# Kernel optimization log

Hardware: AMD Instinct MI355X
Metric: run time of the kernel (lower is better)

## Reference

```python
import jax, jax.numpy as jnp
import numpy as np

T, B, D_IN, H = 1024, 64, 256, 256
D_CAT = D_IN + H  # input to each gate MLP


def setup_inputs() -> dict:
    key = jax.random.key(0)
    k_x, k_w1, k_w2 = jax.random.split(key, 3)
    inputs = jax.random.normal(k_x, (T, B, D_IN), dtype=jnp.float32)
    # 4 gates (forget, input, update, output), weights stacked on leading axis.
    # Layout: W1[g] is (in, out) so combined @ W1[g] + b1[g].
    W1 = jax.random.normal(k_w1, (4, D_CAT, H), dtype=jnp.float32) * (1.0 / np.sqrt(D_CAT))
    b1 = jnp.zeros((4, H), dtype=jnp.float32)
    W2 = jax.random.normal(k_w2, (4, H, H), dtype=jnp.float32) * (1.0 / np.sqrt(H))
    b2 = jnp.zeros((4, H), dtype=jnp.float32)
    return {"inputs": inputs, "W1": W1, "b1": b1, "W2": W2, "b2": b2}


def reference(inputs, W1, b1, W2, b2):
    """HybridQLSTM forward. inputs: [T, B, D_IN]. Returns (stacked [T,B,H], (hx, cx))."""
    Bsz = inputs.shape[1]
    h0 = jnp.zeros((Bsz, H), dtype=inputs.dtype)
    c0 = jnp.zeros((Bsz, H), dtype=inputs.dtype)

    def step(carry, x):
        hx, cx = carry
        combined = jnp.concatenate([x, hx], axis=1)  # [B, D_CAT]
        # All 4 gate MLPs at once: sigmoid(W2 @ tanh(W1 @ combined + b1) + b2)
        hid = jnp.tanh(jnp.einsum('bd,gdh->gbh', combined, W1) + b1[:, None, :])
        gates = jax.nn.sigmoid(jnp.einsum('gbh,ghk->gbk', hid, W2) + b2[:, None, :])
        f, i, u, o = gates[0], gates[1], gates[2], gates[3]
        g = jnp.tanh(u)  # faithful: tanh applied on top of sampler sigmoid
        cx = f * cx + i * g
        hx = o * jnp.tanh(cx)
        return (hx, cx), hx

    (hx, cx), stacked = jax.lax.scan(step, (h0, c0), inputs)
    return stacked, (hx, cx)
```

## Files before the change

### kernel.cpp

```cpp
#include <hip/hip_runtime.h>
#include <math.h>


#define TS    1024
#define NELEM 16384

typedef unsigned long long u64;
typedef unsigned int u32;
typedef unsigned short u16;
typedef _Float16 f16;
typedef __attribute__((ext_vector_type(8))) _Float16 half8;
typedef __attribute__((ext_vector_type(8))) unsigned short ushort8;
typedef __attribute__((ext_vector_type(4))) float f32x4;

__device__ __forceinline__ u64 ld_a8(const u64* p) {
    return __hip_atomic_load(p, __ATOMIC_RELAXED, __HIP_MEMORY_SCOPE_AGENT);
}
__device__ __forceinline__ void st_a8(u64* p, u64 v) {
    __hip_atomic_store(p, v, __ATOMIC_RELAXED, __HIP_MEMORY_SCOPE_AGENT);
}
__device__ __forceinline__ void st_a2(u16* p, u16 v) {
    __hip_atomic_store(p, v, __ATOMIC_RELAXED, __HIP_MEMORY_SCOPE_AGENT);
}

__device__ __forceinline__ void gbar(int e, int bid, int tid, int* flags) {
    __syncthreads();
    if (tid == 0)
        __hip_atomic_store(&flags[bid * 16], e, __ATOMIC_RELAXED, __HIP_MEMORY_SCOPE_AGENT);
    const int l = tid & 63;
    for (;;) {
        int ok = 1;
        if (l < 16) {
            int v = __hip_atomic_load(&flags[l * 16], __ATOMIC_RELAXED, __HIP_MEMORY_SCOPE_AGENT);
            ok = (v >= e);
        }
        if (__all(ok)) break;
        __builtin_amdgcn_s_sleep(1);
    }
    asm volatile("" ::: "memory");
}

__device__ __forceinline__ half8 h8_from(u64 v0, u64 v1) {
    ushort8 t;
#pragma unroll
    for (int q = 0; q < 4; ++q) {
        t[q]     = (u16)(v0 >> (16 * q));
        t[4 + q] = (u16)(v1 >> (16 * q));
    }
    return __builtin_bit_cast(half8, t);
}

__global__ __launch_bounds__(256) void qinit(u64* hglob, int* flags) {
    int i = blockIdx.x * 256 + threadIdx.x;
    st_a8(&hglob[i], 0ull);
    if (i < 16 * 16)
        __hip_atomic_store(&flags[i], 0, __ATOMIC_RELAXED, __HIP_MEMORY_SCOPE_AGENT);
}

__global__ __launch_bounds__(256, 1) void qlstm_persist(
    const float* __restrict__ x,
    const float* __restrict__ W1,
    const float* __restrict__ b1,
    const float* __restrict__ W2,
    const float* __restrict__ b2,
    float* __restrict__ out,
    u64* __restrict__ hglob,
    u16* __restrict__ hidg,
    u16* __restrict__ gateq,
    int* __restrict__ flags)
{
    const int tid = threadIdx.x;
    const int bid = blockIdx.x;
    const int g  = bid >> 2;
    const int ct = bid & 3;

    __shared__ f16 w1s[16 * 4 * 512];
    __shared__ f16 w2s[8 * 4 * 512];
    {
        const float* W1g = W1 + (size_t)g * 512 * 256;
        for (int i = tid; i < 16 * 4 * 64; i += 256) {
            int kt = i >> 8, nt = (i >> 6) & 3, lane = i & 63;
            int k0 = kt * 32 + (lane >> 4) * 8;
            int col = ct * 64 + nt * 16 + (lane & 15);
#pragma unroll
            for (int j = 0; j < 8; ++j)
                w1s[((kt * 4 + nt) * 64 + lane) * 8 + j] = (f16)W1g[(size_t)(k0 + j) * 256 + col];
        }
        const float* W2g = W2 + (size_t)g * 256 * 256;
        for (int i = tid; i < 8 * 4 * 64; i += 256) {
            int kt = i >> 8, nt = (i >> 6) & 3, lane = i & 63;
            int k0 = kt * 32 + (lane >> 4) * 8;
            int col = ct * 64 + nt * 16 + (lane & 15);
#pragma unroll
            for (int j = 0; j < 8; ++j)
                w2s[((kt * 4 + nt) * 64 + lane) * 8 + j] = (f16)W2g[(size_t)(k0 + j) * 256 + col];
        }
        __syncthreads();
    }

    const int l    = tid & 63;
    const int w    = tid >> 6;
    const int quad = l >> 4;
    const int n15  = l & 15;
    const int brow = w * 16 + n15;
    const int bo   = w * 16 + quad * 4;
    float b1v[4], b2v[4];
#pragma unroll
    for (int nt = 0; nt < 4; ++nt) {
        b1v[nt] = b1[g * 256 + ct * 64 + nt * 16 + n15];
        b2v[nt] = b2[g * 256 + ct * 64 + nt * 16 + n15];
    }
    const int e0   = bid * 1024 + tid * 4;
    const int urow = e0 >> 8;
    const int ucol = e0 & 255;
    float creg[4] = {0.f, 0.f, 0.f, 0.f};

    f32x4 acc[4];
#pragma unroll
    for (int nt = 0; nt < 4; ++nt) acc[nt] = (f32x4){0.f, 0.f, 0.f, 0.f};

    {
        const float* xr = x + (size_t)brow * 256;
#pragma unroll
        for (int kt = 0; kt < 8; ++kt) {
            float a[8];
            *(float4*)&a[0] = *(const float4*)(xr + kt * 32 + quad * 8);
            *(float4*)&a[4] = *(const float4*)(xr + kt * 32 + quad * 8 + 4);
            half8 ah;
#pragma unroll
            for (int j = 0; j < 8; ++j) ah[j] = (f16)a[j];
#pragma unroll
            for (int nt = 0; nt < 4; ++nt)
                acc[nt] = __builtin_amdgcn_mfma_f32_16x16x32_f16(
                    ah, *(const half8*)&w1s[((kt * 4 + nt) * 64 + l) * 8], acc[nt], 0, 0, 0);
        }
    }

    for (int t = 0; t < TS; ++t) {
        {
            const u64* hp = hglob + brow * 64;
#pragma unroll
            for (int kt = 8; kt < 16; ++kt) {
                int ko = (kt - 8) * 8 + quad * 2;
                u64 v0 = ld_a8(hp + ko);
                u64 v1 = ld_a8(hp + ko + 1);
                half8 ah = h8_from(v0, v1);
#pragma unroll
                for (int nt = 0; nt < 4; ++nt)
                    acc[nt] = __builtin_amdgcn_mfma_f32_16x16x32_f16(
                        ah, *(const half8*)&w1s[((kt * 4 + nt) * 64 + l) * 8], acc[nt], 0, 0, 0);
            }
        }
#pragma unroll
        for (int nt = 0; nt < 4; ++nt)
#pragma unroll
            for (int r = 0; r < 4; ++r) {
                f16 v = (f16)tanhf(acc[nt][r] + b1v[nt]);
                st_a2(&hidg[(size_t)(g * 64 + bo + r) * 256 + ct * 64 + nt * 16 + n15],
                      __builtin_bit_cast(u16, v));
            }

        gbar(3 * t + 1, bid, tid, flags);

        {
            f32x4 s2[4];
#pragma unroll
            for (int nt = 0; nt < 4; ++nt) s2[nt] = (f32x4){0.f, 0.f, 0.f, 0.f};
            const u64* hr = (const u64*)(hidg + (size_t)(g * 64 + brow) * 256);
#pragma unroll
            for (int kt = 0; kt < 8; ++kt) {
                int ko = kt * 8 + quad * 2;
                u64 v0 = ld_a8(hr + ko);
                u64 v1 = ld_a8(hr + ko + 1);
                half8 ah = h8_from(v0, v1);
#pragma unroll
                for (int nt = 0; nt < 4; ++nt)
                    s2[nt] = __builtin_amdgcn_mfma_f32_16x16x32_f16(
                        ah, *(const half8*)&w2s[((kt * 4 + nt) * 64 + l) * 8], s2[nt], 0, 0, 0);
            }
#pragma unroll
            for (int nt = 0; nt < 4; ++nt)
#pragma unroll
                for (int r = 0; r < 4; ++r) {
                    float sg = 1.0f / (1.0f + expf(-(s2[nt][r] + b2v[nt])));
                    st_a2(&gateq[(size_t)(g * 64 + bo + r) * 256 + ct * 64 + nt * 16 + n15],
                          (u16)(sg * 65535.0f + 0.5f));
                }
        }

        gbar(3 * t + 2, bid, tid, flags);

        {
            const u16* gq = gateq + urow * 256 + ucol;
            u64 qf = ld_a8((const u64*)(gq));
            u64 qi = ld_a8((const u64*)(gq + 16384));
            u64 qu = ld_a8((const u64*)(gq + 32768));
            u64 qo = ld_a8((const u64*)(gq + 49152));
            float4 ov;
            u64 hpack = 0;
            const float s = 1.0f / 65535.0f;
#pragma unroll
            for (int k = 0; k < 4; ++k) {
                float f = (float)((qf >> (16 * k)) & 0xffff) * s;
                float i = (float)((qi >> (16 * k)) & 0xffff) * s;
                float u = (float)((qu >> (16 * k)) & 0xffff) * s;
                float o = (float)((qo >> (16 * k)) & 0xffff) * s;
                creg[k] = f * creg[k] + i * tanhf(u);
                float hn = o * tanhf(creg[k]);
                ((float*)&ov)[k] = hn;
                u16 hb = __builtin_bit_cast(u16, (f16)hn);
                hpack |= (u64)hb << (16 * k);
            }
            *(float4*)(out + (size_t)t * NELEM + e0) = ov;
            st_a8(&hglob[e0 >> 2], hpack);
            if (t == TS - 1) {
                *(float4*)(out + (size_t)TS * NELEM + e0) = ov;
                float4 cv = {creg[0], creg[1], creg[2], creg[3]};
                *(float4*)(out + (size_t)TS * NELEM + NELEM + e0) = cv;
            }
        }

#pragma unroll
        for (int nt = 0; nt < 4; ++nt) acc[nt] = (f32x4){0.f, 0.f, 0.f, 0.f};
        if (t < TS - 1) {
            const float* xr = x + ((size_t)(t + 1) * 64 + brow) * 256;
#pragma unroll
            for (int kt = 0; kt < 8; ++kt) {
                float a[8];
                *(float4*)&a[0] = *(const float4*)(xr + kt * 32 + quad * 8);
                *(float4*)&a[4] = *(const float4*)(xr + kt * 32 + quad * 8 + 4);
                half8 ah;
#pragma unroll
                for (int j = 0; j < 8; ++j) ah[j] = (f16)a[j];
#pragma unroll
                for (int nt = 0; nt < 4; ++nt)
                    acc[nt] = __builtin_amdgcn_mfma_f32_16x16x32_f16(
                        ah, *(const half8*)&w1s[((kt * 4 + nt) * 64 + l) * 8], acc[nt], 0, 0, 0);
            }
        }

        gbar(3 * t + 3, bid, tid, flags);
    }
}

extern "C" void kernel_launch(void* const* d_in, const int* in_sizes, int n_in,
                              void* d_out, int out_size, void* d_ws, size_t ws_size,
                              hipStream_t stream)
{
    const float* x  = (const float*)d_in[0];
    const float* W1 = (const float*)d_in[1];
    const float* b1 = (const float*)d_in[2];
    const float* W2 = (const float*)d_in[3];
    const float* b2 = (const float*)d_in[4];
    float* out = (float*)d_out;

    char* ws = (char*)d_ws;
    u64* hglob = (u64*)ws;
    u16* hidg  = (u16*)(ws + 32768);
    u16* gateq = (u16*)(ws + 32768 + 131072);
    int* flags = (int*)(ws + 32768 + 131072 + 131072);

    qinit<<<16, 256, 0, stream>>>(hglob, flags);
    qlstm_persist<<<16, 256, 0, stream>>>(x, W1, b1, W2, b2, out,
                                          hglob, hidg, gateq, flags);
}
```

Before: 13.43 ms.

## Replace global flag barriers with tagged data words and double-buffered exchange

Removes the three per-step grid-wide flag barriers and instead packs a 16-bit timestep tag into each 64-bit exchanged word. Consumers spin on the data itself until every tag matches. Hidden, gate and h buffers are double-buffered by timestep parity, so producers can run ahead without a trailing barrier. It also switches to fast exp/rcp-based tanh and sigmoid and moves the tanh on the update gate into the producer. The costs are more bytes per exchange (tag overhead) and heavier polling traffic, plus reduced transcendental accuracy.

```diff
diff --git a/kernel.cpp b/kernel.cpp
--- a/kernel.cpp
+++ b/kernel.cpp
@@ -10,7 +10,6 @@
 typedef unsigned short u16;
 typedef _Float16 f16;
 typedef __attribute__((ext_vector_type(8))) _Float16 half8;
-typedef __attribute__((ext_vector_type(8))) unsigned short ushort8;
 typedef __attribute__((ext_vector_type(4))) float f32x4;
 
 __device__ __forceinline__ u64 ld_a8(const u64* p) {
@@ -19,42 +18,19 @@
 __device__ __forceinline__ void st_a8(u64* p, u64 v) {
     __hip_atomic_store(p, v, __ATOMIC_RELAXED, __HIP_MEMORY_SCOPE_AGENT);
 }
-__device__ __forceinline__ void st_a2(u16* p, u16 v) {
-    __hip_atomic_store(p, v, __ATOMIC_RELAXED, __HIP_MEMORY_SCOPE_AGENT);
-}
-
-__device__ __forceinline__ void gbar(int e, int bid, int tid, int* flags) {
-    __syncthreads();
-    if (tid == 0)
-        __hip_atomic_store(&flags[bid * 16], e, __ATOMIC_RELAXED, __HIP_MEMORY_SCOPE_AGENT);
-    const int l = tid & 63;
-    for (;;) {
-        int ok = 1;
-        if (l < 16) {
-            int v = __hip_atomic_load(&flags[l * 16], __ATOMIC_RELAXED, __HIP_MEMORY_SCOPE_AGENT);
-            ok = (v >= e);
-        }
-        if (__all(ok)) break;
-        __builtin_amdgcn_s_sleep(1);
-    }
-    asm volatile("" ::: "memory");
-}
-
-__device__ __forceinline__ half8 h8_from(u64 v0, u64 v1) {
-    ushort8 t;
-#pragma unroll
-    for (int q = 0; q < 4; ++q) {
-        t[q]     = (u16)(v0 >> (16 * q));
-        t[4 + q] = (u16)(v1 >> (16 * q));
-    }
-    return __builtin_bit_cast(half8, t);
-}
-
-__global__ __launch_bounds__(256) void qinit(u64* hglob, int* flags) {
-    int i = blockIdx.x * 256 + threadIdx.x;
-    st_a8(&hglob[i], 0ull);
-    if (i < 16 * 16)
-        __hip_atomic_store(&flags[i], 0, __ATOMIC_RELAXED, __HIP_MEMORY_SCOPE_AGENT);
+
+__device__ __forceinline__ float fast_tanh(float xx) {
+    float e = __expf(2.0f * xx);
+    return 1.0f - 2.0f * __builtin_amdgcn_rcpf(e + 1.0f);
+}
+__device__ __forceinline__ float fast_sig(float xx) {
+    return __builtin_amdgcn_rcpf(1.0f + __expf(-xx));
+}
+
+__global__ __launch_bounds__(256) void qinit(u64* ws64, int n) {
+    int stride = gridDim.x * 256;
+    for (int i = blockIdx.x * 256 + threadIdx.x; i < n; i += stride)
+        st_a8(&ws64[i], 0ull);
 }
 
 __global__ __launch_bounds__(256, 1) void qlstm_persist(
@@ -64,10 +40,9 @@
     const float* __restrict__ W2,
     const float* __restrict__ b2,
     float* __restrict__ out,
-    u64* __restrict__ hglob,
-    u16* __restrict__ hidg,
-    u16* __restrict__ gateq,
-    int* __restrict__ flags)
+    u64* __restrict__ h64,
+    u64* __restrict__ hid64,
+    u64* __restrict__ gat64)
 {
     const int tid = threadIdx.x;
     const int bid = blockIdx.x;
@@ -138,81 +113,141 @@
 
     for (int t = 0; t < TS; ++t) {
         {
-            const u64* hp = hglob + brow * 64;
-#pragma unroll
-            for (int kt = 8; kt < 16; ++kt) {
-                int ko = (kt - 8) * 8 + quad * 2;
-                u64 v0 = ld_a8(hp + ko);
-                u64 v1 = ld_a8(hp + ko + 1);
-                half8 ah = h8_from(v0, v1);
+            const u64* hb = h64 + (size_t)(t & 1) * 8192 + (size_t)brow * 128;
+            const u16 wantH = (u16)t;
+            u64 hv[32];
+            for (;;) {
+                bool ok = true;
+#pragma unroll
+                for (int i = 0; i < 32; ++i) {
+                    int kt = i >> 2, j = i & 3;
+                    hv[i] = ld_a8(hb + kt * 16 + quad * 4 + j);
+                }
+#pragma unroll
+                for (int i = 0; i < 32; ++i) ok &= ((u16)(hv[i] >> 48) == wantH);
+                if (__all(ok)) break;
+            }
+#pragma unroll
+            for (int kt = 0; kt < 8; ++kt) {
+                half8 ah;
+#pragma unroll
+                for (int j = 0; j < 4; ++j) {
+                    u64 v = hv[kt * 4 + j];
+                    ah[2 * j]     = __builtin_bit_cast(f16, (u16)v);
+                    ah[2 * j + 1] = __builtin_bit_cast(f16, (u16)(v >> 32));
+                }
 #pragma unroll
                 for (int nt = 0; nt < 4; ++nt)
                     acc[nt] = __builtin_amdgcn_mfma_f32_16x16x32_f16(
-                        ah, *(const half8*)&w1s[((kt * 4 + nt) * 64 + l) * 8], acc[nt], 0, 0, 0);
-            }
-        }
-#pragma unroll
-        for (int nt = 0; nt < 4; ++nt)
-#pragma unroll
-            for (int r = 0; r < 4; ++r) {
-                f16 v = (f16)tanhf(acc[nt][r] + b1v[nt]);
-                st_a2(&hidg[(size_t)(g * 64 + bo + r) * 256 + ct * 64 + nt * 16 + n15],
-                      __builtin_bit_cast(u16, v));
-            }
-
-        gbar(3 * t + 1, bid, tid, flags);
+                        ah, *(const half8*)&w1s[(((kt + 8) * 4 + nt) * 64 + l) * 8], acc[nt], 0, 0, 0);
+            }
+        }
+
+        {
+            u64* hd = hid64 + (size_t)(t & 1) * 32768;
+            const u64 tagw = (u64)(u16)(t + 1) << 48;
+#pragma unroll
+            for (int nt = 0; nt < 4; ++nt)
+#pragma unroll
+                for (int r = 0; r < 4; ++r) {
+                    f16 v = (f16)fast_tanh(acc[nt][r] + b1v[nt]);
+                    u32 pv = (u32)__builtin_bit_cast(u16, v);
+                    u32 po = (u32)__shfl_xor((int)pv, 1);
+                    if ((n15 & 1) == 0) {
+                        int cp = ct * 32 + nt * 8 + (n15 >> 1);
+                        st_a8(&hd[(size_t)(g * 64 + bo + r) * 128 + cp],
+                              tagw | ((u64)po << 32) | pv);
+                    }
+                }
+        }
 
         {
             f32x4 s2[4];
 #pragma unroll
             for (int nt = 0; nt < 4; ++nt) s2[nt] = (f32x4){0.f, 0.f, 0.f, 0.f};
-            const u64* hr = (const u64*)(hidg + (size_t)(g * 64 + brow) * 256);
+            const u64* hr = hid64 + (size_t)(t & 1) * 32768 + (size_t)(g * 64 + brow) * 128;
+            const u16 wantM = (u16)(t + 1);
+            u64 mv[32];
+            for (;;) {
+                bool ok = true;
+#pragma unroll
+                for (int i = 0; i < 32; ++i) {
+                    int kt = i >> 2, j = i & 3;
+                    mv[i] = ld_a8(hr + kt * 16 + quad * 4 + j);
+                }
+#pragma unroll
+                for (int i = 0; i < 32; ++i) ok &= ((u16)(mv[i] >> 48) == wantM);
+                if (__all(ok)) break;
+            }
 #pragma unroll
             for (int kt = 0; kt < 8; ++kt) {
-                int ko = kt * 8 + quad * 2;
-                u64 v0 = ld_a8(hr + ko);
-                u64 v1 = ld_a8(hr + ko + 1);
-                half8 ah = h8_from(v0, v1);
+                half8 ah;
+#pragma unroll
+                for (int j = 0; j < 4; ++j) {
+                    u64 v = mv[kt * 4 + j];
+                    ah[2 * j]     = __builtin_bit_cast(f16, (u16)v);
+                    ah[2 * j + 1] = __builtin_bit_cast(f16, (u16)(v >> 32));
+                }
 #pragma unroll
                 for (int nt = 0; nt < 4; ++nt)
                     s2[nt] = __builtin_amdgcn_mfma_f32_16x16x32_f16(
                         ah, *(const half8*)&w2s[((kt * 4 + nt) * 64 + l) * 8], s2[nt], 0, 0, 0);
             }
+            u64* gd = gat64 + (size_t)(t & 1) * 32768;
+            const u64 tagw = (u64)(u16)(t + 1) << 48;
 #pragma unroll
             for (int nt = 0; nt < 4; ++nt)
 #pragma unroll
                 for (int r = 0; r < 4; ++r) {
-                    float sg = 1.0f / (1.0f + expf(-(s2[nt][r] + b2v[nt])));
-                    st_a2(&gateq[(size_t)(g * 64 + bo + r) * 256 + ct * 64 + nt * 16 + n15],
-                          (u16)(sg * 65535.0f + 0.5f));
-                }
-        }
-
-        gbar(3 * t + 2, bid, tid, flags);
-
-        {
-            const u16* gq = gateq + urow * 256 + ucol;
-            u64 qf = ld_a8((const u64*)(gq));
-            u64 qi = ld_a8((const u64*)(gq + 16384));
-            u64 qu = ld_a8((const u64*)(gq + 32768));
-            u64 qo = ld_a8((const u64*)(gq + 49152));
+                    float sg = fast_sig(s2[nt][r] + b2v[nt]);
+                    if (g == 2) sg = fast_tanh(sg);
+                    u32 q  = (u32)(sg * 65535.0f + 0.5f);
+                    u32 oq = (u32)__shfl_xor((int)q, 1);
+                    if ((n15 & 1) == 0) {
+                        int cp = ct * 32 + nt * 8 + (n15 >> 1);
+                        st_a8(&gd[(size_t)(g * 64 + bo + r) * 128 + cp],
+                              tagw | ((u64)oq << 16) | q);
+                    }
+                }
+        }
+
+        {
+            const u64* gb = gat64 + (size_t)(t & 1) * 32768 + (size_t)urow * 128 + (ucol >> 1);
+            const u16 wantG = (u16)(t + 1);
+            u64 gv[8];
+            for (;;) {
+                bool ok = true;
+#pragma unroll
+                for (int gg = 0; gg < 4; ++gg) {
+                    gv[gg * 2]     = ld_a8(gb + gg * 8192);
+                    gv[gg * 2 + 1] = ld_a8(gb + gg * 8192 + 1);
+                }
+#pragma unroll
+                for (int i = 0; i < 8; ++i) ok &= ((u16)(gv[i] >> 48) == wantG);
+                if (__all(ok)) break;
+            }
             float4 ov;
-            u64 hpack = 0;
             const float s = 1.0f / 65535.0f;
+            u64* hw = h64 + (size_t)((t + 1) & 1) * 8192;
+            const u64 tagH = (u64)(u16)(t + 1) << 48;
+            u64 hp[2];
 #pragma unroll
             for (int k = 0; k < 4; ++k) {
-                float f = (float)((qf >> (16 * k)) & 0xffff) * s;
-                float i = (float)((qi >> (16 * k)) & 0xffff) * s;
-                float u = (float)((qu >> (16 * k)) & 0xffff) * s;
-                float o = (float)((qo >> (16 * k)) & 0xffff) * s;
-                creg[k] = f * creg[k] + i * tanhf(u);
-                float hn = o * tanhf(creg[k]);
+                int wsel = k >> 1, sh = 16 * (k & 1);
+                float f  = (float)((gv[0 + wsel] >> sh) & 0xffff) * s;
+                float i  = (float)((gv[2 + wsel] >> sh) & 0xffff) * s;
+                float gu = (float)((gv[4 + wsel] >> sh) & 0xffff) * s;
+                float o  = (float)((gv[6 + wsel] >> sh) & 0xffff) * s;
+                creg[k] = f * creg[k] + i * gu;
+                float hn = o * fast_tanh(creg[k]);
                 ((float*)&ov)[k] = hn;
-                u16 hb = __builtin_bit_cast(u16, (f16)hn);
-                hpack |= (u64)hb << (16 * k);
+                u64 hb16 = (u64)__builtin_bit_cast(u16, (f16)hn);
+                if ((k & 1) == 0) hp[k >> 1] = tagH | hb16;
+                else              hp[k >> 1] |= (hb16 << 32);
             }
             *(float4*)(out + (size_t)t * NELEM + e0) = ov;
-            st_a8(&hglob[e0 >> 2], hpack);
+            st_a8(&hw[urow * 128 + (ucol >> 1)],     hp[0]);
+            st_a8(&hw[urow * 128 + (ucol >> 1) + 1], hp[1]);
             if (t == TS - 1) {
                 *(float4*)(out + (size_t)TS * NELEM + e0) = ov;
                 float4 cv = {creg[0], creg[1], creg[2], creg[3]};
@@ -238,8 +273,6 @@
                         ah, *(const half8*)&w1s[((kt * 4 + nt) * 64 + l) * 8], acc[nt], 0, 0, 0);
             }
         }
-
-        gbar(3 * t + 3, bid, tid, flags);
     }
 }
 
@@ -255,12 +288,11 @@
     float* out = (float*)d_out;
 
     char* ws = (char*)d_ws;
-    u64* hglob = (u64*)ws;
-    u16* hidg  = (u16*)(ws + 32768);
-    u16* gateq = (u16*)(ws + 32768 + 131072);
-    int* flags = (int*)(ws + 32768 + 131072 + 131072);
-
-    qinit<<<16, 256, 0, stream>>>(hglob, flags);
+    u64* h64   = (u64*)ws;
+    u64* hid64 = (u64*)(ws + 131072);
+    u64* gat64 = (u64*)(ws + 131072 + 524288);
+
+    qinit<<<64, 256, 0, stream>>>((u64*)ws, 147456);
     qlstm_persist<<<16, 256, 0, stream>>>(x, W1, b1, W2, b2, out,
-                                          hglob, hidg, gateq, flags);
-}
+                                          h64, hid64, gat64);
+}
```

After: 23.97 ms. 78.5% more time.

## Repartition blocks by hidden column across all gates to drop one grid barrier per step

Applied to the files above, without the earlier changes.

Each of the 16 blocks now owns 16 hidden columns for all four gates instead of 64 columns of one gate. The LSTM cell update can then run right after the second MLP layer without a global exchange of quantized gate values, so each timestep needs two grid barriers instead of three. Hidden activations are transposed in-register with shuffles and stored as packed 64-bit words, and the second-layer loads are batched before the MFMAs. tanh and sigmoid use fast exp/rcp approximations, and the 16-bit gate quantization is removed, with some small accuracy tradeoffs.

```diff
diff --git a/kernel.cpp b/kernel.cpp
--- a/kernel.cpp
+++ b/kernel.cpp
@@ -19,8 +19,13 @@
 __device__ __forceinline__ void st_a8(u64* p, u64 v) {
     __hip_atomic_store(p, v, __ATOMIC_RELAXED, __HIP_MEMORY_SCOPE_AGENT);
 }
-__device__ __forceinline__ void st_a2(u16* p, u16 v) {
-    __hip_atomic_store(p, v, __ATOMIC_RELAXED, __HIP_MEMORY_SCOPE_AGENT);
+
+__device__ __forceinline__ float fast_tanh(float xx) {
+    float e = __expf(2.0f * xx);
+    return 1.0f - 2.0f * __builtin_amdgcn_rcpf(e + 1.0f);
+}
+__device__ __forceinline__ float fast_sig(float xx) {
+    return __builtin_amdgcn_rcpf(1.0f + __expf(-xx));
 }
 
 __device__ __forceinline__ void gbar(int e, int bid, int tid, int* flags) {
@@ -50,11 +55,33 @@
     return __builtin_bit_cast(half8, t);
 }
 
-__global__ __launch_bounds__(256) void qinit(u64* hglob, int* flags) {
+__device__ __forceinline__ void xpose4(float v[4], int p) {
+#pragma unroll
+    for (int m = 1; m <= 2; m <<= 1) {
+        float nv[4];
+#pragma unroll
+        for (int r = 0; r < 4; ++r) {
+            float ex = __shfl_xor(v[r ^ m], m);
+            nv[r] = ((r ^ p) & m) ? ex : v[r];
+        }
+#pragma unroll
+        for (int r = 0; r < 4; ++r) v[r] = nv[r];
+    }
+}
+
+__device__ __forceinline__ u64 pk4f16(const float v[4]) {
+    u64 r = 0;
+#pragma unroll
+    for (int k = 0; k < 4; ++k)
+        r |= (u64)__builtin_bit_cast(u16, (f16)v[k]) << (16 * k);
+    return r;
+}
+
+__global__ __launch_bounds__(256) void qinit(u64* h64, int* flags) {
     int i = blockIdx.x * 256 + threadIdx.x;
-    st_a8(&hglob[i], 0ull);
-    if (i < 16 * 16)
-        __hip_atomic_store(&flags[i], 0, __ATOMIC_RELAXED, __HIP_MEMORY_SCOPE_AGENT);
+    st_a8(&h64[i], 0ull);
+    if (i < 128)
+        st_a8((u64*)flags + i, 0ull);
 }
 
 __global__ __launch_bounds__(256, 1) void qlstm_persist(
@@ -64,36 +91,34 @@
     const float* __restrict__ W2,
     const float* __restrict__ b2,
     float* __restrict__ out,
-    u64* __restrict__ hglob,
-    u16* __restrict__ hidg,
-    u16* __restrict__ gateq,
+    u64* __restrict__ h64,
+    u64* __restrict__ hid64,
     int* __restrict__ flags)
 {
     const int tid = threadIdx.x;
     const int bid = blockIdx.x;
-    const int g  = bid >> 2;
-    const int ct = bid & 3;
+    const int ct = bid;
 
     __shared__ f16 w1s[16 * 4 * 512];
     __shared__ f16 w2s[8 * 4 * 512];
     {
-        const float* W1g = W1 + (size_t)g * 512 * 256;
         for (int i = tid; i < 16 * 4 * 64; i += 256) {
-            int kt = i >> 8, nt = (i >> 6) & 3, lane = i & 63;
+            int kt = i >> 8, g = (i >> 6) & 3, lane = i & 63;
             int k0 = kt * 32 + (lane >> 4) * 8;
-            int col = ct * 64 + nt * 16 + (lane & 15);
+            int col = ct * 16 + (lane & 15);
+            const float* W1g = W1 + (size_t)g * 512 * 256;
 #pragma unroll
             for (int j = 0; j < 8; ++j)
-                w1s[((kt * 4 + nt) * 64 + lane) * 8 + j] = (f16)W1g[(size_t)(k0 + j) * 256 + col];
-        }
-        const float* W2g = W2 + (size_t)g * 256 * 256;
+                w1s[(size_t)i * 8 + j] = (f16)W1g[(size_t)(k0 + j) * 256 + col];
+        }
         for (int i = tid; i < 8 * 4 * 64; i += 256) {
-            int kt = i >> 8, nt = (i >> 6) & 3, lane = i & 63;
+            int kt = i >> 8, g = (i >> 6) & 3, lane = i & 63;
             int k0 = kt * 32 + (lane >> 4) * 8;
-            int col = ct * 64 + nt * 16 + (lane & 15);
+            int col = ct * 16 + (lane & 15);
+            const float* W2g = W2 + (size_t)g * 256 * 256;
 #pragma unroll
             for (int j = 0; j < 8; ++j)
-                w2s[((kt * 4 + nt) * 64 + lane) * 8 + j] = (f16)W2g[(size_t)(k0 + j) * 256 + col];
+                w2s[(size_t)i * 8 + j] = (f16)W2g[(size_t)(k0 + j) * 256 + col];
         }
         __syncthreads();
     }
@@ -104,20 +129,20 @@
     const int n15  = l & 15;
     const int brow = w * 16 + n15;
     const int bo   = w * 16 + quad * 4;
+    const int p    = l & 3;
+    const int cq   = ct * 4 + (n15 >> 2);
+    const int cbase = ct * 16 + (n15 & ~3);
     float b1v[4], b2v[4];
 #pragma unroll
-    for (int nt = 0; nt < 4; ++nt) {
-        b1v[nt] = b1[g * 256 + ct * 64 + nt * 16 + n15];
-        b2v[nt] = b2[g * 256 + ct * 64 + nt * 16 + n15];
-    }
-    const int e0   = bid * 1024 + tid * 4;
-    const int urow = e0 >> 8;
-    const int ucol = e0 & 255;
+    for (int g = 0; g < 4; ++g) {
+        b1v[g] = b1[g * 256 + ct * 16 + n15];
+        b2v[g] = b2[g * 256 + ct * 16 + n15];
+    }
     float creg[4] = {0.f, 0.f, 0.f, 0.f};
 
     f32x4 acc[4];
 #pragma unroll
-    for (int nt = 0; nt < 4; ++nt) acc[nt] = (f32x4){0.f, 0.f, 0.f, 0.f};
+    for (int g = 0; g < 4; ++g) acc[g] = (f32x4){0.f, 0.f, 0.f, 0.f};
 
     {
         const float* xr = x + (size_t)brow * 256;
@@ -130,98 +155,92 @@
 #pragma unroll
             for (int j = 0; j < 8; ++j) ah[j] = (f16)a[j];
 #pragma unroll
-            for (int nt = 0; nt < 4; ++nt)
-                acc[nt] = __builtin_amdgcn_mfma_f32_16x16x32_f16(
-                    ah, *(const half8*)&w1s[((kt * 4 + nt) * 64 + l) * 8], acc[nt], 0, 0, 0);
+            for (int g = 0; g < 4; ++g)
+                acc[g] = __builtin_amdgcn_mfma_f32_16x16x32_f16(
+                    ah, *(const half8*)&w1s[((kt * 4 + g) * 64 + l) * 8], acc[g], 0, 0, 0);
         }
     }
 
     for (int t = 0; t < TS; ++t) {
         {
-            const u64* hp = hglob + brow * 64;
-#pragma unroll
-            for (int kt = 8; kt < 16; ++kt) {
-                int ko = (kt - 8) * 8 + quad * 2;
-                u64 v0 = ld_a8(hp + ko);
-                u64 v1 = ld_a8(hp + ko + 1);
-                half8 ah = h8_from(v0, v1);
-#pragma unroll
-                for (int nt = 0; nt < 4; ++nt)
-                    acc[nt] = __builtin_amdgcn_mfma_f32_16x16x32_f16(
-                        ah, *(const half8*)&w1s[((kt * 4 + nt) * 64 + l) * 8], acc[nt], 0, 0, 0);
-            }
-        }
-#pragma unroll
-        for (int nt = 0; nt < 4; ++nt)
-#pragma unroll
-            for (int r = 0; r < 4; ++r) {
-                f16 v = (f16)tanhf(acc[nt][r] + b1v[nt]);
-                st_a2(&hidg[(size_t)(g * 64 + bo + r) * 256 + ct * 64 + nt * 16 + n15],
-                      __builtin_bit_cast(u16, v));
-            }
-
-        gbar(3 * t + 1, bid, tid, flags);
-
-        {
-            f32x4 s2[4];
-#pragma unroll
-            for (int nt = 0; nt < 4; ++nt) s2[nt] = (f32x4){0.f, 0.f, 0.f, 0.f};
-            const u64* hr = (const u64*)(hidg + (size_t)(g * 64 + brow) * 256);
+            const u64* hp = h64 + (size_t)brow * 64;
+            u64 hv[16];
 #pragma unroll
             for (int kt = 0; kt < 8; ++kt) {
                 int ko = kt * 8 + quad * 2;
-                u64 v0 = ld_a8(hr + ko);
-                u64 v1 = ld_a8(hr + ko + 1);
-                half8 ah = h8_from(v0, v1);
-#pragma unroll
-                for (int nt = 0; nt < 4; ++nt)
-                    s2[nt] = __builtin_amdgcn_mfma_f32_16x16x32_f16(
-                        ah, *(const half8*)&w2s[((kt * 4 + nt) * 64 + l) * 8], s2[nt], 0, 0, 0);
-            }
-#pragma unroll
-            for (int nt = 0; nt < 4; ++nt)
-#pragma unroll
-                for (int r = 0; r < 4; ++r) {
-                    float sg = 1.0f / (1.0f + expf(-(s2[nt][r] + b2v[nt])));
-                    st_a2(&gateq[(size_t)(g * 64 + bo + r) * 256 + ct * 64 + nt * 16 + n15],
-                          (u16)(sg * 65535.0f + 0.5f));
+                hv[kt * 2]     = ld_a8(hp + ko);
+                hv[kt * 2 + 1] = ld_a8(hp + ko + 1);
+            }
+#pragma unroll
+            for (int kt = 0; kt < 8; ++kt) {
+                half8 ah = h8_from(hv[kt * 2], hv[kt * 2 + 1]);
+#pragma unroll
+                for (int g = 0; g < 4; ++g)
+                    acc[g] = __builtin_amdgcn_mfma_f32_16x16x32_f16(
+                        ah, *(const half8*)&w1s[(((kt + 8) * 4 + g) * 64 + l) * 8], acc[g], 0, 0, 0);
+            }
+        }
+
+#pragma unroll
+        for (int g = 0; g < 4; ++g) {
+            float mv[4];
+#pragma unroll
+            for (int r = 0; r < 4; ++r) mv[r] = fast_tanh(acc[g][r] + b1v[g]);
+            xpose4(mv, p);
+            st_a8(&hid64[(size_t)(g * 64 + bo + p) * 64 + cq], pk4f16(mv));
+        }
+
+        gbar(2 * t + 1, bid, tid, flags);
+
+        f32x4 s2[4];
+#pragma unroll
+        for (int g = 0; g < 4; ++g) s2[g] = (f32x4){0.f, 0.f, 0.f, 0.f};
+        {
+            u64 mv[64];
+#pragma unroll
+            for (int kt = 0; kt < 8; ++kt)
+#pragma unroll
+                for (int g = 0; g < 4; ++g) {
+                    const u64* hr = hid64 + (size_t)(g * 64 + brow) * 64 + kt * 8 + quad * 2;
+                    mv[(kt * 4 + g) * 2]     = ld_a8(hr);
+                    mv[(kt * 4 + g) * 2 + 1] = ld_a8(hr + 1);
                 }
-        }
-
-        gbar(3 * t + 2, bid, tid, flags);
+#pragma unroll
+            for (int kt = 0; kt < 8; ++kt)
+#pragma unroll
+                for (int g = 0; g < 4; ++g) {
+                    half8 ah = h8_from(mv[(kt * 4 + g) * 2], mv[(kt * 4 + g) * 2 + 1]);
+                    s2[g] = __builtin_amdgcn_mfma_f32_16x16x32_f16(
+                        ah, *(const half8*)&w2s[((kt * 4 + g) * 64 + l) * 8], s2[g], 0, 0, 0);
+                }
+        }
 
         {
-            const u16* gq = gateq + urow * 256 + ucol;
-            u64 qf = ld_a8((const u64*)(gq));
-            u64 qi = ld_a8((const u64*)(gq + 16384));
-            u64 qu = ld_a8((const u64*)(gq + 32768));
-            u64 qo = ld_a8((const u64*)(gq + 49152));
-            float4 ov;
-            u64 hpack = 0;
-            const float s = 1.0f / 65535.0f;
-#pragma unroll
-            for (int k = 0; k < 4; ++k) {
-                float f = (float)((qf >> (16 * k)) & 0xffff) * s;
-                float i = (float)((qi >> (16 * k)) & 0xffff) * s;
-                float u = (float)((qu >> (16 * k)) & 0xffff) * s;
-                float o = (float)((qo >> (16 * k)) & 0xffff) * s;
-                creg[k] = f * creg[k] + i * tanhf(u);
-                float hn = o * tanhf(creg[k]);
-                ((float*)&ov)[k] = hn;
-                u16 hb = __builtin_bit_cast(u16, (f16)hn);
-                hpack |= (u64)hb << (16 * k);
-            }
-            *(float4*)(out + (size_t)t * NELEM + e0) = ov;
-            st_a8(&hglob[e0 >> 2], hpack);
+            float hn[4];
+#pragma unroll
+            for (int r = 0; r < 4; ++r) {
+                float f  = fast_sig(s2[0][r] + b2v[0]);
+                float ig = fast_sig(s2[1][r] + b2v[1]);
+                float ug = fast_tanh(fast_sig(s2[2][r] + b2v[2]));
+                float og = fast_sig(s2[3][r] + b2v[3]);
+                creg[r] = f * creg[r] + ig * ug;
+                hn[r] = og * fast_tanh(creg[r]);
+            }
+            xpose4(hn, p);
+            float4 ov = {hn[0], hn[1], hn[2], hn[3]};
+            *(float4*)(out + (size_t)t * NELEM + (size_t)(bo + p) * 256 + cbase) = ov;
+            st_a8(&h64[(size_t)(bo + p) * 64 + cq], pk4f16(hn));
             if (t == TS - 1) {
-                *(float4*)(out + (size_t)TS * NELEM + e0) = ov;
-                float4 cv = {creg[0], creg[1], creg[2], creg[3]};
-                *(float4*)(out + (size_t)TS * NELEM + NELEM + e0) = cv;
-            }
-        }
-
-#pragma unroll
-        for (int nt = 0; nt < 4; ++nt) acc[nt] = (f32x4){0.f, 0.f, 0.f, 0.f};
+                *(float4*)(out + (size_t)TS * NELEM + (size_t)(bo + p) * 256 + cbase) = ov;
+                float cv[4] = {creg[0], creg[1], creg[2], creg[3]};
+                xpose4(cv, p);
+                float4 cvv = {cv[0], cv[1], cv[2], cv[3]};
+                *(float4*)(out + (size_t)TS * NELEM + NELEM + (size_t)(bo + p) * 256 + cbase) = cvv;
+            }
+        }
+
+#pragma unroll
+        for (int g = 0; g < 4; ++g) acc[g] = (f32x4){0.f, 0.f, 0.f, 0.f};
         if (t < TS - 1) {
             const float* xr = x + ((size_t)(t + 1) * 64 + brow) * 256;
 #pragma unroll
@@ -233,13 +252,13 @@
 #pragma unroll
                 for (int j = 0; j < 8; ++j) ah[j] = (f16)a[j];
 #pragma unroll
-                for (int nt = 0; nt < 4; ++nt)
-                    acc[nt] = __builtin_amdgcn_mfma_f32_16x16x32_f16(
-                        ah, *(const half8*)&w1s[((kt * 4 + nt) * 64 + l) * 8], acc[nt], 0, 0, 0);
-            }
-        }
-
-        gbar(3 * t + 3, bid, tid, flags);
+                for (int g = 0; g < 4; ++g)
+                    acc[g] = __builtin_amdgcn_mfma_f32_16x16x32_f16(
+                        ah, *(const half8*)&w1s[((kt * 4 + g) * 64 + l) * 8], acc[g], 0, 0, 0);
+            }
+        }
+
+        gbar(2 * t + 2, bid, tid, flags);
     }
 }
 
@@ -255,12 +274,11 @@
     float* out = (float*)d_out;
 
     char* ws = (char*)d_ws;
-    u64* hglob = (u64*)ws;
-    u16* hidg  = (u16*)(ws + 32768);
-    u16* gateq = (u16*)(ws + 32768 + 131072);
-    int* flags = (int*)(ws + 32768 + 131072 + 131072);
-
-    qinit<<<16, 256, 0, stream>>>(hglob, flags);
+    u64* h64   = (u64*)ws;
+    u64* hid64 = (u64*)(ws + 32768);
+    int* flags = (int*)(ws + 32768 + 131072);
+
+    qinit<<<16, 256, 0, stream>>>(h64, flags);
     qlstm_persist<<<16, 256, 0, stream>>>(x, W1, b1, W2, b2, out,
-                                          hglob, hidg, gateq, flags);
-}
+                                          h64, hid64, flags);
+}
```

Result: slower. 14.55 ms (+8.4%).

## Pack gate/hidden exchanges into 64-bit stores via lane transposes, use fast transcendentals

Applied to the files above, without the earlier changes.

Replaces the per-element 16-bit atomic stores of hidden activations and quantized gates with a 4x4 register transpose across lanes, so each lane writes one packed 64-bit value. It also swaps tanhf/expf for exp+rcp approximations and moves the tanh on the update gate into the gate producer blocks. The global barrier now packs its flags densely, spins in only one wave and ends with a block sync. Recurrent h loads are batched ahead of the MFMA chain. The aim is fewer global transactions and shorter latency on each step's critical path, at the cost of some accuracy from the approximate transcendentals.

```diff
diff --git a/kernel.cpp b/kernel.cpp
--- a/kernel.cpp
+++ b/kernel.cpp
@@ -19,24 +19,31 @@
 __device__ __forceinline__ void st_a8(u64* p, u64 v) {
     __hip_atomic_store(p, v, __ATOMIC_RELAXED, __HIP_MEMORY_SCOPE_AGENT);
 }
-__device__ __forceinline__ void st_a2(u16* p, u16 v) {
-    __hip_atomic_store(p, v, __ATOMIC_RELAXED, __HIP_MEMORY_SCOPE_AGENT);
+
+__device__ __forceinline__ float fast_tanh(float xx) {
+    float e = __expf(2.0f * xx);
+    return 1.0f - 2.0f * __builtin_amdgcn_rcpf(e + 1.0f);
+}
+__device__ __forceinline__ float fast_sig(float xx) {
+    return __builtin_amdgcn_rcpf(1.0f + __expf(-xx));
 }
 
 __device__ __forceinline__ void gbar(int e, int bid, int tid, int* flags) {
     __syncthreads();
     if (tid == 0)
-        __hip_atomic_store(&flags[bid * 16], e, __ATOMIC_RELAXED, __HIP_MEMORY_SCOPE_AGENT);
-    const int l = tid & 63;
-    for (;;) {
-        int ok = 1;
-        if (l < 16) {
-            int v = __hip_atomic_load(&flags[l * 16], __ATOMIC_RELAXED, __HIP_MEMORY_SCOPE_AGENT);
-            ok = (v >= e);
-        }
-        if (__all(ok)) break;
-        __builtin_amdgcn_s_sleep(1);
-    }
+        __hip_atomic_store(&flags[bid], e, __ATOMIC_RELAXED, __HIP_MEMORY_SCOPE_AGENT);
+    if (tid < 64) {
+        for (;;) {
+            int ok = 1;
+            if (tid < 16) {
+                int v = __hip_atomic_load(&flags[tid], __ATOMIC_RELAXED, __HIP_MEMORY_SCOPE_AGENT);
+                ok = (v >= e);
+            }
+            if (__all(ok)) break;
+            __builtin_amdgcn_s_sleep(1);
+        }
+    }
+    __syncthreads();
     asm volatile("" ::: "memory");
 }
 
@@ -50,10 +57,40 @@
     return __builtin_bit_cast(half8, t);
 }
 
-__global__ __launch_bounds__(256) void qinit(u64* hglob, int* flags) {
+__device__ __forceinline__ void xpose4(float v[4], int p) {
+#pragma unroll
+    for (int m = 1; m <= 2; m <<= 1) {
+        float nv[4];
+#pragma unroll
+        for (int r = 0; r < 4; ++r) {
+            float ex = __shfl_xor(v[r ^ m], m);
+            nv[r] = ((r ^ p) & m) ? ex : v[r];
+        }
+#pragma unroll
+        for (int r = 0; r < 4; ++r) v[r] = nv[r];
+    }
+}
+
+__device__ __forceinline__ u64 pk4f16(const float v[4]) {
+    u64 r = 0;
+#pragma unroll
+    for (int k = 0; k < 4; ++k)
+        r |= (u64)__builtin_bit_cast(u16, (f16)v[k]) << (16 * k);
+    return r;
+}
+
+__device__ __forceinline__ u64 pk4q16(const float v[4]) {
+    u64 r = 0;
+#pragma unroll
+    for (int k = 0; k < 4; ++k)
+        r |= (u64)(u16)(v[k] * 65535.0f + 0.5f) << (16 * k);
+    return r;
+}
+
+__global__ __launch_bounds__(256) void qinit(u64* h64, int* flags) {
     int i = blockIdx.x * 256 + threadIdx.x;
-    st_a8(&hglob[i], 0ull);
-    if (i < 16 * 16)
+    st_a8(&h64[i], 0ull);
+    if (i < 16)
         __hip_atomic_store(&flags[i], 0, __ATOMIC_RELAXED, __HIP_MEMORY_SCOPE_AGENT);
 }
 
@@ -64,9 +101,9 @@
     const float* __restrict__ W2,
     const float* __restrict__ b2,
     float* __restrict__ out,
-    u64* __restrict__ hglob,
-    u16* __restrict__ hidg,
-    u16* __restrict__ gateq,
+    u64* __restrict__ h64,
+    u64* __restrict__ hid64,
+    u64* __restrict__ gat64,
     int* __restrict__ flags)
 {
     const int tid = threadIdx.x;
@@ -84,7 +121,7 @@
             int col = ct * 64 + nt * 16 + (lane & 15);
 #pragma unroll
             for (int j = 0; j < 8; ++j)
-                w1s[((kt * 4 + nt) * 64 + lane) * 8 + j] = (f16)W1g[(size_t)(k0 + j) * 256 + col];
+                w1s[(size_t)i * 8 + j] = (f16)W1g[(size_t)(k0 + j) * 256 + col];
         }
         const float* W2g = W2 + (size_t)g * 256 * 256;
         for (int i = tid; i < 8 * 4 * 64; i += 256) {
@@ -93,7 +130,7 @@
             int col = ct * 64 + nt * 16 + (lane & 15);
 #pragma unroll
             for (int j = 0; j < 8; ++j)
-                w2s[((kt * 4 + nt) * 64 + lane) * 8 + j] = (f16)W2g[(size_t)(k0 + j) * 256 + col];
+                w2s[(size_t)i * 8 + j] = (f16)W2g[(size_t)(k0 + j) * 256 + col];
         }
         __syncthreads();
     }
@@ -104,6 +141,8 @@
     const int n15  = l & 15;
     const int brow = w * 16 + n15;
     const int bo   = w * 16 + quad * 4;
+    const int p    = l & 3;
+    const int cqb  = ct * 16 + (n15 >> 2);
     float b1v[4], b2v[4];
 #pragma unroll
     for (int nt = 0; nt < 4; ++nt) {
@@ -112,7 +151,7 @@
     }
     const int e0   = bid * 1024 + tid * 4;
     const int urow = e0 >> 8;
-    const int ucol = e0 & 255;
+    const int ucq  = (e0 & 255) >> 2;
     float creg[4] = {0.f, 0.f, 0.f, 0.f};
 
     f32x4 acc[4];
@@ -138,27 +177,32 @@
 
     for (int t = 0; t < TS; ++t) {
         {
-            const u64* hp = hglob + brow * 64;
-#pragma unroll
-            for (int kt = 8; kt < 16; ++kt) {
-                int ko = (kt - 8) * 8 + quad * 2;
-                u64 v0 = ld_a8(hp + ko);
-                u64 v1 = ld_a8(hp + ko + 1);
-                half8 ah = h8_from(v0, v1);
+            const u64* hp = h64 + (size_t)brow * 64;
+            u64 hv[16];
+#pragma unroll
+            for (int kt = 0; kt < 8; ++kt) {
+                int ko = kt * 8 + quad * 2;
+                hv[kt * 2]     = ld_a8(hp + ko);
+                hv[kt * 2 + 1] = ld_a8(hp + ko + 1);
+            }
+#pragma unroll
+            for (int kt = 0; kt < 8; ++kt) {
+                half8 ah = h8_from(hv[kt * 2], hv[kt * 2 + 1]);
 #pragma unroll
                 for (int nt = 0; nt < 4; ++nt)
                     acc[nt] = __builtin_amdgcn_mfma_f32_16x16x32_f16(
-                        ah, *(const half8*)&w1s[((kt * 4 + nt) * 64 + l) * 8], acc[nt], 0, 0, 0);
-            }
-        }
-#pragma unroll
-        for (int nt = 0; nt < 4; ++nt)
-#pragma unroll
-            for (int r = 0; r < 4; ++r) {
-                f16 v = (f16)tanhf(acc[nt][r] + b1v[nt]);
-                st_a2(&hidg[(size_t)(g * 64 + bo + r) * 256 + ct * 64 + nt * 16 + n15],
-                      __builtin_bit_cast(u16, v));
-            }
+                        ah, *(const half8*)&w1s[(((kt + 8) * 4 + nt) * 64 + l) * 8], acc[nt], 0, 0, 0);
+            }
+        }
+
+#pragma unroll
+        for (int nt = 0; nt < 4; ++nt) {
+            float mv[4];
+#pragma unroll
+            for (int r = 0; r < 4; ++r) mv[r] = fast_tanh(acc[nt][r] + b1v[nt]);
+            xpose4(mv, p);
+            st_a8(&hid64[(size_t)(g * 64 + bo + p) * 64 + cqb + nt * 4], pk4f16(mv));
+        }
 
         gbar(3 * t + 1, bid, tid, flags);
 
@@ -166,53 +210,59 @@
             f32x4 s2[4];
 #pragma unroll
             for (int nt = 0; nt < 4; ++nt) s2[nt] = (f32x4){0.f, 0.f, 0.f, 0.f};
-            const u64* hr = (const u64*)(hidg + (size_t)(g * 64 + brow) * 256);
+            const u64* hr = hid64 + (size_t)(g * 64 + brow) * 64;
+            u64 mv2[16];
 #pragma unroll
             for (int kt = 0; kt < 8; ++kt) {
                 int ko = kt * 8 + quad * 2;
-                u64 v0 = ld_a8(hr + ko);
-                u64 v1 = ld_a8(hr + ko + 1);
-                half8 ah = h8_from(v0, v1);
+                mv2[kt * 2]     = ld_a8(hr + ko);
+                mv2[kt * 2 + 1] = ld_a8(hr + ko + 1);
+            }
+#pragma unroll
+            for (int kt = 0; kt < 8; ++kt) {
+                half8 ah = h8_from(mv2[kt * 2], mv2[kt * 2 + 1]);
 #pragma unroll
                 for (int nt = 0; nt < 4; ++nt)
                     s2[nt] = __builtin_amdgcn_mfma_f32_16x16x32_f16(
                         ah, *(const half8*)&w2s[((kt * 4 + nt) * 64 + l) * 8], s2[nt], 0, 0, 0);
             }
 #pragma unroll
-            for (int nt = 0; nt < 4; ++nt)
+            for (int nt = 0; nt < 4; ++nt) {
+                float gv[4];
 #pragma unroll
                 for (int r = 0; r < 4; ++r) {
-                    float sg = 1.0f / (1.0f + expf(-(s2[nt][r] + b2v[nt])));
-                    st_a2(&gateq[(size_t)(g * 64 + bo + r) * 256 + ct * 64 + nt * 16 + n15],
-                          (u16)(sg * 65535.0f + 0.5f));
+                    float sg = fast_sig(s2[nt][r] + b2v[nt]);
+                    if (g == 2) sg = fast_tanh(sg);
+                    gv[r] = sg;
                 }
+                xpose4(gv, p);
+                st_a8(&gat64[(size_t)(g * 64 + bo + p) * 64 + cqb + nt * 4], pk4q16(gv));
+            }
         }
 
         gbar(3 * t + 2, bid, tid, flags);
 
         {
-            const u16* gq = gateq + urow * 256 + ucol;
-            u64 qf = ld_a8((const u64*)(gq));
-            u64 qi = ld_a8((const u64*)(gq + 16384));
-            u64 qu = ld_a8((const u64*)(gq + 32768));
-            u64 qo = ld_a8((const u64*)(gq + 49152));
+            u64 qf = ld_a8(&gat64[(size_t)(0 * 64 + urow) * 64 + ucq]);
+            u64 qi = ld_a8(&gat64[(size_t)(1 * 64 + urow) * 64 + ucq]);
+            u64 qu = ld_a8(&gat64[(size_t)(2 * 64 + urow) * 64 + ucq]);
+            u64 qo = ld_a8(&gat64[(size_t)(3 * 64 + urow) * 64 + ucq]);
             float4 ov;
             u64 hpack = 0;
             const float s = 1.0f / 65535.0f;
 #pragma unroll
             for (int k = 0; k < 4; ++k) {
-                float f = (float)((qf >> (16 * k)) & 0xffff) * s;
-                float i = (float)((qi >> (16 * k)) & 0xffff) * s;
-                float u = (float)((qu >> (16 * k)) & 0xffff) * s;
-                float o = (float)((qo >> (16 * k)) & 0xffff) * s;
-                creg[k] = f * creg[k] + i * tanhf(u);
-                float hn = o * tanhf(creg[k]);
+                float f  = (float)((qf >> (16 * k)) & 0xffff) * s;
+                float ig = (float)((qi >> (16 * k)) & 0xffff) * s;
+                float ug = (float)((qu >> (16 * k)) & 0xffff) * s;
+                float og = (float)((qo >> (16 * k)) & 0xffff) * s;
+                creg[k] = f * creg[k] + ig * ug;
+                float hn = og * fast_tanh(creg[k]);
                 ((float*)&ov)[k] = hn;
-                u16 hb = __builtin_bit_cast(u16, (f16)hn);
-                hpack |= (u64)hb << (16 * k);
+                hpack |= (u64)__builtin_bit_cast(u16, (f16)hn) << (16 * k);
             }
             *(float4*)(out + (size_t)t * NELEM + e0) = ov;
-            st_a8(&hglob[e0 >> 2], hpack);
+            st_a8(&h64[(size_t)urow * 64 + ucq], hpack);
             if (t == TS - 1) {
                 *(float4*)(out + (size_t)TS * NELEM + e0) = ov;
                 float4 cv = {creg[0], creg[1], creg[2], creg[3]};
@@ -255,12 +305,12 @@
     float* out = (float*)d_out;
 
     char* ws = (char*)d_ws;
-    u64* hglob = (u64*)ws;
-    u16* hidg  = (u16*)(ws + 32768);
-    u16* gateq = (u16*)(ws + 32768 + 131072);
+    u64* h64   = (u64*)ws;
+    u64* hid64 = (u64*)(ws + 32768);
+    u64* gat64 = (u64*)(ws + 32768 + 131072);
     int* flags = (int*)(ws + 32768 + 131072 + 131072);
 
-    qinit<<<16, 256, 0, stream>>>(hglob, flags);
+    qinit<<<16, 256, 0, stream>>>(h64, flags);
     qlstm_persist<<<16, 256, 0, stream>>>(x, W1, b1, W2, b2, out,
-                                          hglob, hidg, gateq, flags);
-}
+                                          h64, hid64, gat64, flags);
+}
```

Measured after the change: 12.61 ms. -6.0%, faster.
